# Kernel tuning notes

Hardware: AMD Instinct MI355X
Metric: run time of the kernel (lower is better)

## Reference

```python
import jax, jax.numpy as jnp
import numpy as np

NUM_USERS = 100000
NUM_ITEMS = 50000
EMBED_DIM = 64
N_LAYERS = 3
NUM_EDGES = 3276800  # avg user degree 32
BATCH = 16384


def setup_inputs() -> dict:
    key = jax.random.key(0)
    k0, k1, k2, k3, k4, k5 = jax.random.split(key, 6)
    rows = jax.random.randint(k0, (NUM_EDGES,), 0, NUM_USERS, dtype=jnp.int32)
    cols = jax.random.randint(k1, (NUM_EDGES,), 0, NUM_ITEMS, dtype=jnp.int32)
    user_table = jax.random.normal(k2, (NUM_USERS, EMBED_DIM), dtype=jnp.float32) * 0.1
    item_table = jax.random.normal(k3, (NUM_ITEMS, EMBED_DIM), dtype=jnp.float32) * 0.1
    user_indices = jax.random.randint(k4, (BATCH,), 0, NUM_USERS, dtype=jnp.int32)
    item_indices = jax.random.randint(k5, (BATCH,), 0, NUM_ITEMS, dtype=jnp.int32)
    return {
        "user_table": user_table,
        "item_table": item_table,
        "rows": rows,
        "cols": cols,
        "user_indices": user_indices,
        "item_indices": item_indices,
    }


def reference(user_table, item_table, rows, cols, user_indices, item_indices):
    # D^-1 A row-normalization of the binary bipartite adjacency:
    # normalized edge value for edge (u, i) is 1 / deg(u) (0 if isolated).
    ones = jnp.ones(rows.shape, dtype=user_table.dtype)
    deg = jax.ops.segment_sum(ones, rows, num_segments=NUM_USERS)
    inv_deg = jnp.where(deg > 0, 1.0 / deg, 0.0)
    vals = inv_deg[rows]  # [E]

    u = user_table  # [U, D] (unused by propagation in the original too)
    it = item_table  # [I, D]
    for _ in range(N_LAYERS):
        # u = A @ it  (SpMM via gather + segment-sum over destination users)
        u = jax.ops.segment_sum(vals[:, None] * it[cols], rows, num_segments=NUM_USERS)
        # it = A^T @ u
        it = jax.ops.segment_sum(vals[:, None] * u[rows], cols, num_segments=NUM_ITEMS)

    scores = jnp.sum(u[user_indices] * it[item_indices], axis=-1)  # [B]
    return jax.nn.sigmoid(scores)
```

## Files before the change

kernel.cpp:

```cpp
#include <hip/hip_runtime.h>
#include <math.h>

#define NUM_USERS 100000
#define NUM_ITEMS 50000
#define EMBED     64
#define NUM_EDGES 3276800
#define BATCH     16384
#define CAP       10752
#define NBUCK     391
#define NBUCK_I   391
#define P1_EDGES  16384
#define P1_THREADS 512
#define CVT_BLOCKS 1563

typedef _Float16 half8 __attribute__((ext_vector_type(8)));

__global__ void prep_kernel(const float* __restrict__ itab, _Float16* __restrict__ it16,
                            int* __restrict__ curzero,
                            _Float16* __restrict__ w16) {
    int b = blockIdx.x;
    if (b < CVT_BLOCKS) {
        int i = b * 256 + threadIdx.x;
        if (i < NUM_ITEMS * EMBED / 8) {
            const float4* p = (const float4*)itab + 2 * i;
            float4 a = p[0], c = p[1];
            half8 o;
            o[0] = (_Float16)a.x; o[1] = (_Float16)a.y; o[2] = (_Float16)a.z; o[3] = (_Float16)a.w;
            o[4] = (_Float16)c.x; o[5] = (_Float16)c.y; o[6] = (_Float16)c.z; o[7] = (_Float16)c.w;
            ((half8*)it16)[i] = o;
        }
    } else if (b == CVT_BLOCKS) {
        for (int k = threadIdx.x; k < 800; k += 256) curzero[k] = 0;
    } else {
        int i = threadIdx.x;
        if (i < 64) w16[(long long)NUM_USERS * EMBED + i] = (_Float16)0.f;
        else if (i < 128) it16[(long long)NUM_ITEMS * EMBED + (i - 64)] = (_Float16)0.f;
    }
}

__global__ void __launch_bounds__(P1_THREADS)
pass1_kernel(const int* __restrict__ rows, const int* __restrict__ cols,
             int* __restrict__ ucur, int* __restrict__ icur,
             int* __restrict__ rec_u, int* __restrict__ rec_i) {
    __shared__ int hu[400], hi[400], gu[400], gi[400];
    __shared__ int lbase[400], lcur[400];
    __shared__ int sc[512];
    __shared__ int recbuf[P1_EDGES];
    int t = threadIdx.x;
    long long e0 = (long long)blockIdx.x * P1_EDGES;

    int er[32], ec[32];
    #pragma unroll
    for (int q = 0; q < 32; ++q) {
        er[q] = rows[e0 + t + q * P1_THREADS];
        ec[q] = cols[e0 + t + q * P1_THREADS];
    }

    for (int i = t; i < 400; i += P1_THREADS) { hu[i] = 0; hi[i] = 0; }
    __syncthreads();
    #pragma unroll
    for (int q = 0; q < 32; ++q) {
        atomicAdd(&hu[er[q] >> 8], 1);
        atomicAdd(&hi[ec[q] >> 7], 1);
    }
    __syncthreads();
    for (int i = t; i < 400; i += P1_THREADS) {
        int vr = (hu[i] + 15) & ~15;
        gu[i] = vr ? atomicAdd(&ucur[i], vr) : 0;
        vr = (hi[i] + 15) & ~15;
        gi[i] = vr ? atomicAdd(&icur[i], vr) : 0;
    }

    __syncthreads();
    sc[t] = (t < 400) ? hu[t] : 0;
    __syncthreads();
    for (int o = 1; o < 512; o <<= 1) {
        int x = (t >= o) ? sc[t - o] : 0; __syncthreads();
        sc[t] += x; __syncthreads();
    }
    if (t < 400) { lbase[t] = sc[t] - hu[t]; lcur[t] = 0; }
    __syncthreads();
    #pragma unroll
    for (int q = 0; q < 32; ++q) {
        int b = er[q] >> 8;
        int p = lbase[b] + atomicAdd(&lcur[b], 1);
        recbuf[p] = (ec[q] << 8) | (er[q] & 255);
    }
    __syncthreads();
    sc[t] = (t < 400) ? ((hu[t] + 15) & ~15) : 0;
    __syncthreads();
    for (int o = 1; o < 512; o <<= 1) {
        int x = (t >= o) ? sc[t - o] : 0; __syncthreads();
        sc[t] += x; __syncthreads();
    }
    int total = sc[511];
    for (int o4 = t * 4; o4 < total; o4 += P1_THREADS * 4) {
        int lo = 0, hi_ = 399;
        while (lo < hi_) { int mid = (lo + hi_) >> 1; if (sc[mid] > o4) hi_ = mid; else lo = mid + 1; }
        int b = lo;
        int v = hu[b];
        int vr = (v + 15) & ~15;
        int j = o4 - (sc[b] - vr);
        int gpos = gu[b] + j;
        if (gpos + 3 < CAP) {
            int4 val;
            val.x = (j + 0 < v) ? recbuf[lbase[b] + j + 0] : -1;
            val.y = (j + 1 < v) ? recbuf[lbase[b] + j + 1] : -1;
            val.z = (j + 2 < v) ? recbuf[lbase[b] + j + 2] : -1;
            val.w = (j + 3 < v) ? recbuf[lbase[b] + j + 3] : -1;
            *(int4*)(rec_u + (long long)b * CAP + gpos) = val;
        } else {
            for (int k = 0; k < 4; ++k)
                if (gpos + k < CAP)
                    rec_u[(long long)b * CAP + gpos + k] = (j + k < v) ? recbuf[lbase[b] + j + k] : -1;
        }
    }

    __syncthreads();
    sc[t] = (t < 400) ? hi[t] : 0;
    __syncthreads();
    for (int o = 1; o < 512; o <<= 1) {
        int x = (t >= o) ? sc[t - o] : 0; __syncthreads();
        sc[t] += x; __syncthreads();
    }
    if (t < 400) { lbase[t] = sc[t] - hi[t]; lcur[t] = 0; }
    __syncthreads();
    #pragma unroll
    for (int q = 0; q < 32; ++q) {
        int b = ec[q] >> 7;
        int p = lbase[b] + atomicAdd(&lcur[b], 1);
        recbuf[p] = (er[q] << 7) | (ec[q] & 127);
    }
    __syncthreads();
    sc[t] = (t < 400) ? ((hi[t] + 15) & ~15) : 0;
    __syncthreads();
    for (int o = 1; o < 512; o <<= 1) {
        int x = (t >= o) ? sc[t - o] : 0; __syncthreads();
        sc[t] += x; __syncthreads();
    }
    total = sc[511];
    for (int o4 = t * 4; o4 < total; o4 += P1_THREADS * 4) {
        int lo = 0, hi_ = 399;
        while (lo < hi_) { int mid = (lo + hi_) >> 1; if (sc[mid] > o4) hi_ = mid; else lo = mid + 1; }
        int b = lo;
        int v = hi[b];
        int vr = (v + 15) & ~15;
        int j = o4 - (sc[b] - vr);
        int gpos = gi[b] + j;
        if (gpos + 3 < CAP) {
            int4 val;
            val.x = (j + 0 < v) ? recbuf[lbase[b] + j + 0] : -1;
            val.y = (j + 1 < v) ? recbuf[lbase[b] + j + 1] : -1;
            val.z = (j + 2 < v) ? recbuf[lbase[b] + j + 2] : -1;
            val.w = (j + 3 < v) ? recbuf[lbase[b] + j + 3] : -1;
            *(int4*)(rec_i + (long long)b * CAP + gpos) = val;
        } else {
            for (int k = 0; k < 4; ++k)
                if (gpos + k < CAP)
                    rec_i[(long long)b * CAP + gpos + k] = (j + k < v) ? recbuf[lbase[b] + j + k] : -1;
        }
    }
}

template <int VBITS>
__device__ __forceinline__ void pass2_body(int* __restrict__ rec, const int* __restrict__ cur,
                                           int* __restrict__ deg, int* __restrict__ off,
                                           float* __restrict__ inv32, int ncap, int b,
                                           int* buf, int* h, int* ex, int* cnt, int* sc) {
    const int V = 1 << VBITS, M = V - 1;
    int t = threadIdx.x;
    long long s = (long long)b * CAP;
    int n = cur[b]; if (n > CAP) n = CAP;
    for (int i = t; i < n; i += 256) buf[i] = rec[s + i];
    if (t < V) { h[t] = 0; cnt[t] = 0; }
    __syncthreads();
    for (int i = t; i < n; i += 256) {
        int r = buf[i];
        if (r != -1) atomicAdd(&h[r & M], 1);
    }
    __syncthreads();
    if (t < V) sc[t] = h[t];
    __syncthreads();
    for (int o = 1; o < V; o <<= 1) {
        int x = (t >= o && t < V) ? sc[t - o] : 0;
        __syncthreads();
        if (t < V) sc[t] += x;
        __syncthreads();
    }
    if (t < V) {
        ex[t] = sc[t] - h[t];
        int id = b * V + t;
        if (id < ncap) {
            int v = h[t];
            deg[id] = v;
            off[id] = (int)(s + ex[t]);
            if (inv32) inv32[id] = v ? 1.0f / (float)v : 0.0f;
        }
    }
    __syncthreads();
    for (int i = t; i < n; i += 256) {
        int r = buf[i];
        if (r == -1) continue;
        int k = r & M;
        int rnk = atomicAdd(&cnt[k], 1);
        rec[s + ex[k] + rnk] = (int)(((unsigned)r) >> VBITS);
    }
}

__global__ void __launch_bounds__(256)
pass2_kernel(int* __restrict__ rec_u, const int* __restrict__ ucur,
             int* __restrict__ udeg, int* __restrict__ uoff, float* __restrict__ inv32,
             int* __restrict__ rec_i, const int* __restrict__ icur,
             int* __restrict__ ideg, int* __restrict__ ioff) {
    __shared__ int buf[CAP];
    __shared__ int h[256], ex[256], cnt[256], sc[256];
    if (blockIdx.x < NBUCK)
        pass2_body<8>(rec_u, ucur, udeg, uoff, inv32, NUM_USERS, blockIdx.x,
                      buf, h, ex, cnt, sc);
    else
        pass2_body<7>(rec_i, icur, ideg, ioff, (float*)nullptr, NUM_ITEMS,
                      blockIdx.x - NBUCK, buf, h, ex, cnt, sc);
}

__global__ void gather_u(const int* __restrict__ uoff, const int* __restrict__ udeg,
                         const int* __restrict__ csr_col, const float* __restrict__ inv32,
                         const _Float16* __restrict__ it, _Float16* __restrict__ w) {
    int row = blockIdx.x * 4 + (threadIdx.x >> 6);
    if (row >= NUM_USERS) return;
    int lane = threadIdx.x & 63;
    int slot = lane >> 3;
    int h    = lane & 7;
    int start = uoff[row];
    int end = start + udeg[row];
    half8 acc = {0, 0, 0, 0, 0, 0, 0, 0};
    for (int k = start; k < end; k += 32) {
        int e1 = end - 1;
        int i0 = k + slot, i1 = i0 + 8, i2 = i0 + 16, i3 = i0 + 24;
        int c0 = csr_col[i0 < e1 ? i0 : e1];
        int c1 = csr_col[i1 < e1 ? i1 : e1];
        int c2 = csr_col[i2 < e1 ? i2 : e1];
        int c3 = csr_col[i3 < e1 ? i3 : e1];
        c0 = i0 < end ? c0 : NUM_ITEMS;
        c1 = i1 < end ? c1 : NUM_ITEMS;
        c2 = i2 < end ? c2 : NUM_ITEMS;
        c3 = i3 < end ? c3 : NUM_ITEMS;
        half8 x0 = *(const half8*)(it + (long long)c0 * EMBED + (h << 3));
        half8 x1 = *(const half8*)(it + (long long)c1 * EMBED + (h << 3));
        half8 x2 = *(const half8*)(it + (long long)c2 * EMBED + (h << 3));
        half8 x3 = *(const half8*)(it + (long long)c3 * EMBED + (h << 3));
        acc += x0; acc += x1; acc += x2; acc += x3;
    }
    float f[8];
    #pragma unroll
    for (int j = 0; j < 8; ++j) {
        f[j] = (float)acc[j];
        f[j] += __shfl_xor(f[j], 8, 64);
        f[j] += __shfl_xor(f[j], 16, 64);
        f[j] += __shfl_xor(f[j], 32, 64);
    }
    if (lane < 8) {
        float v = inv32[row];
        float v2 = v * v;
        half8 ow;
        #pragma unroll
        for (int j = 0; j < 8; ++j) ow[j] = (_Float16)(f[j] * v2);
        *(half8*)(w + (long long)row * EMBED + (lane << 3)) = ow;
    }
}

__device__ __forceinline__ void gather_it_body(int col, int lane,
                                               const int* __restrict__ ioff,
                                               const int* __restrict__ ideg,
                                               const int* __restrict__ csc_row,
                                               const _Float16* __restrict__ w,
                                               _Float16* __restrict__ it) {
    int slot = lane >> 3;
    int h    = lane & 7;
    int start = ioff[col];
    int end = start + ideg[col];
    half8 acc = {0, 0, 0, 0, 0, 0, 0, 0};
    for (int k = start; k < end; k += 64) {
        int e1 = end - 1;
        int idx[8], r[8];
        #pragma unroll
        for (int q = 0; q < 8; ++q) {
            idx[q] = k + slot + q * 8;
            int safe = idx[q] < e1 ? idx[q] : e1;
            r[q] = csc_row[safe];
            r[q] = idx[q] < end ? r[q] : NUM_USERS;
        }
        half8 x[8];
        #pragma unroll
        for (int q = 0; q < 8; ++q)
            x[q] = *(const half8*)(w + (long long)r[q] * EMBED + (h << 3));
        #pragma unroll
        for (int q = 0; q < 8; ++q) acc += x[q];
    }
    float f[8];
    #pragma unroll
    for (int j = 0; j < 8; ++j) {
        f[j] = (float)acc[j];
        f[j] += __shfl_xor(f[j], 8, 64);
        f[j] += __shfl_xor(f[j], 16, 64);
        f[j] += __shfl_xor(f[j], 32, 64);
    }
    if (lane < 8) {
        half8 o;
        #pragma unroll
        for (int j = 0; j < 8; ++j) o[j] = (_Float16)f[j];
        *(half8*)(it + (long long)col * EMBED + (lane << 3)) = o;
    }
}

__global__ void gather_it(const int* __restrict__ ioff, const int* __restrict__ ideg,
                          const int* __restrict__ csc_row,
                          const _Float16* __restrict__ w, _Float16* __restrict__ it) {
    int col = blockIdx.x * 4 + (threadIdx.x >> 6);
    if (col >= NUM_ITEMS) return;
    gather_it_body(col, threadIdx.x & 63, ioff, ideg, csc_row, w, it);
}

__global__ void gather_it_batch(const int* __restrict__ ioff, const int* __restrict__ ideg,
                                const int* __restrict__ csc_row,
                                const _Float16* __restrict__ w, _Float16* __restrict__ it,
                                const int* __restrict__ iidx) {
    int b = blockIdx.x * 4 + (threadIdx.x >> 6);
    if (b >= BATCH) return;
    gather_it_body(iidx[b], threadIdx.x & 63, ioff, ideg, csc_row, w, it);
}

__global__ void score_kernel(const _Float16* __restrict__ w, const _Float16* __restrict__ it,
                             const int* __restrict__ udeg,
                             const int* __restrict__ uidx, const int* __restrict__ iidx,
                             float* __restrict__ out) {
    int wave_in_block = threadIdx.x >> 6;
    int lane = threadIdx.x & 63;
    int b = blockIdx.x * 4 + wave_in_block;
    if (b >= BATCH) return;
    int ui = uidx[b];
    int ii = iidx[b];
    float s = (float)w[(long long)ui * EMBED + lane] * (float)it[(long long)ii * EMBED + lane];
    #pragma unroll
    for (int off = 32; off > 0; off >>= 1)
        s += __shfl_down(s, off, 64);
    if (lane == 0) {
        s *= (float)udeg[ui];
        out[b] = 1.0f / (1.0f + expf(-s));
    }
}

extern "C" void kernel_launch(void* const* d_in, const int* in_sizes, int n_in,
                              void* d_out, int out_size, void* d_ws, size_t ws_size,
                              hipStream_t stream) {
    const float* item_table = (const float*)d_in[1];
    const int*   rows       = (const int*)d_in[2];
    const int*   cols       = (const int*)d_in[3];
    const int*   uidx       = (const int*)d_in[4];
    const int*   iidx       = (const int*)d_in[5];
    float* out = (float*)d_out;

    char* base = (char*)d_ws;
    int*   udeg  = (int*)(base + 0);
    int*   ideg  = (int*)(base +   400000);
    int*   uoff  = (int*)(base +   600000);
    int*   ioff  = (int*)(base +  1000000);
    float* inv32 = (float*)(base + 1200000);
    int*   ucur  = (int*)(base +  1600000);
    int*   icur  = (int*)(base +  1601600);
    int*   rec_u = (int*)(base +  1720320);
    int*   rec_i = (int*)(base + 18923520);
    _Float16* w16  = (_Float16*)(base + 36126720);
    _Float16* it16 = (_Float16*)(base + 48926848);

    prep_kernel<<<CVT_BLOCKS + 2, 256, 0, stream>>>(item_table, it16, ucur, w16);

    pass1_kernel<<<NUM_EDGES / P1_EDGES, P1_THREADS, 0, stream>>>(
        rows, cols, ucur, icur, rec_u, rec_i);
    pass2_kernel<<<NBUCK + NBUCK_I, 256, 0, stream>>>(rec_u, ucur, udeg, uoff, inv32,
                                                      rec_i, icur, ideg, ioff);

    const int ublocks = (NUM_USERS + 3) / 4;
    const int iblocks = (NUM_ITEMS + 3) / 4;
    for (int l = 0; l < 3; ++l) {
        gather_u<<<ublocks, 256, 0, stream>>>(uoff, udeg, rec_u, inv32, it16, w16);
        if (l < 2)
            gather_it<<<iblocks, 256, 0, stream>>>(ioff, ideg, rec_i, w16, it16);
        else
            gather_it_batch<<<BATCH / 4, 256, 0, stream>>>(ioff, ideg, rec_i, w16, it16, iidx);
    }

    score_kernel<<<BATCH / 4, 256, 0, stream>>>(w16, it16, udeg, uidx, iidx, out);
}
```

Baseline: 431.8 us.

## Split item embeddings into column halves and fuse final item gather with scoring

Stores the fp16 item table as two 32-wide halves, and runs the user gather twice, once per half. Each pass gathers a 3.2 MB working set that is more likely to stay in cache. The last-layer item gather is merged with the score computation, so the item rows for the batch are no longer written and re-read. The cost is twice as many user-gather launches and a second read of the CSR indices.

```diff
diff --git a/kernel.cpp b/kernel.cpp
--- a/kernel.cpp
+++ b/kernel.cpp
@@ -8,33 +8,37 @@
 #define BATCH     16384
 #define CAP       10752
 #define NBUCK     391
-#define NBUCK_I   391
 #define P1_EDGES  16384
 #define P1_THREADS 512
-#define CVT_BLOCKS 1563
+#define CVT_GROUPS (NUM_ITEMS * 8)
+#define CVT_BLOCKS ((CVT_GROUPS + 255) / 256)
 
 typedef _Float16 half8 __attribute__((ext_vector_type(8)));
 
-__global__ void prep_kernel(const float* __restrict__ itab, _Float16* __restrict__ it16,
-                            int* __restrict__ curzero,
-                            _Float16* __restrict__ w16) {
+__global__ void prep_kernel(const float* __restrict__ itab,
+                            _Float16* __restrict__ it_lo, _Float16* __restrict__ it_hi,
+                            int* __restrict__ curzero, _Float16* __restrict__ w16) {
     int b = blockIdx.x;
     if (b < CVT_BLOCKS) {
         int i = b * 256 + threadIdx.x;
-        if (i < NUM_ITEMS * EMBED / 8) {
+        if (i < CVT_GROUPS) {
+            int row = i >> 3, g = i & 7;
             const float4* p = (const float4*)itab + 2 * i;
             float4 a = p[0], c = p[1];
             half8 o;
             o[0] = (_Float16)a.x; o[1] = (_Float16)a.y; o[2] = (_Float16)a.z; o[3] = (_Float16)a.w;
             o[4] = (_Float16)c.x; o[5] = (_Float16)c.y; o[6] = (_Float16)c.z; o[7] = (_Float16)c.w;
-            ((half8*)it16)[i] = o;
+            _Float16* dst = (g < 4) ? (it_lo + (long long)row * 32 + g * 8)
+                                    : (it_hi + (long long)row * 32 + (g - 4) * 8);
+            *(half8*)dst = o;
         }
     } else if (b == CVT_BLOCKS) {
         for (int k = threadIdx.x; k < 800; k += 256) curzero[k] = 0;
     } else {
         int i = threadIdx.x;
-        if (i < 64) w16[(long long)NUM_USERS * EMBED + i] = (_Float16)0.f;
-        else if (i < 128) it16[(long long)NUM_ITEMS * EMBED + (i - 64)] = (_Float16)0.f;
+        if (i < 32) it_lo[(long long)NUM_ITEMS * 32 + i] = (_Float16)0.f;
+        else if (i < 64) it_hi[(long long)NUM_ITEMS * 32 + (i - 32)] = (_Float16)0.f;
+        else if (i < 128) w16[(long long)NUM_USERS * EMBED + (i - 64)] = (_Float16)0.f;
     }
 }
 
@@ -222,20 +226,21 @@
                       blockIdx.x - NBUCK, buf, h, ex, cnt, sc);
 }
 
-__global__ void gather_u(const int* __restrict__ uoff, const int* __restrict__ udeg,
-                         const int* __restrict__ csr_col, const float* __restrict__ inv32,
-                         const _Float16* __restrict__ it, _Float16* __restrict__ w) {
+__global__ void gather_u_half(const int* __restrict__ uoff, const int* __restrict__ udeg,
+                              const int* __restrict__ csr_col, const float* __restrict__ inv32,
+                              const _Float16* __restrict__ itH,
+                              _Float16* __restrict__ w, int halfofs) {
     int row = blockIdx.x * 4 + (threadIdx.x >> 6);
     if (row >= NUM_USERS) return;
     int lane = threadIdx.x & 63;
-    int slot = lane >> 3;
-    int h    = lane & 7;
+    int slot = lane >> 2;
+    int d    = lane & 3;
     int start = uoff[row];
     int end = start + udeg[row];
     half8 acc = {0, 0, 0, 0, 0, 0, 0, 0};
-    for (int k = start; k < end; k += 32) {
+    for (int k = start; k < end; k += 64) {
         int e1 = end - 1;
-        int i0 = k + slot, i1 = i0 + 8, i2 = i0 + 16, i3 = i0 + 24;
+        int i0 = k + slot, i1 = i0 + 16, i2 = i0 + 32, i3 = i0 + 48;
         int c0 = csr_col[i0 < e1 ? i0 : e1];
         int c1 = csr_col[i1 < e1 ? i1 : e1];
         int c2 = csr_col[i2 < e1 ? i2 : e1];
@@ -244,36 +249,37 @@
         c1 = i1 < end ? c1 : NUM_ITEMS;
         c2 = i2 < end ? c2 : NUM_ITEMS;
         c3 = i3 < end ? c3 : NUM_ITEMS;
-        half8 x0 = *(const half8*)(it + (long long)c0 * EMBED + (h << 3));
-        half8 x1 = *(const half8*)(it + (long long)c1 * EMBED + (h << 3));
-        half8 x2 = *(const half8*)(it + (long long)c2 * EMBED + (h << 3));
-        half8 x3 = *(const half8*)(it + (long long)c3 * EMBED + (h << 3));
+        half8 x0 = *(const half8*)(itH + (long long)c0 * 32 + (d << 3));
+        half8 x1 = *(const half8*)(itH + (long long)c1 * 32 + (d << 3));
+        half8 x2 = *(const half8*)(itH + (long long)c2 * 32 + (d << 3));
+        half8 x3 = *(const half8*)(itH + (long long)c3 * 32 + (d << 3));
         acc += x0; acc += x1; acc += x2; acc += x3;
     }
     float f[8];
     #pragma unroll
     for (int j = 0; j < 8; ++j) {
         f[j] = (float)acc[j];
+        f[j] += __shfl_xor(f[j], 4, 64);
         f[j] += __shfl_xor(f[j], 8, 64);
         f[j] += __shfl_xor(f[j], 16, 64);
         f[j] += __shfl_xor(f[j], 32, 64);
     }
-    if (lane < 8) {
+    if (lane < 4) {
         float v = inv32[row];
         float v2 = v * v;
         half8 ow;
         #pragma unroll
         for (int j = 0; j < 8; ++j) ow[j] = (_Float16)(f[j] * v2);
-        *(half8*)(w + (long long)row * EMBED + (lane << 3)) = ow;
-    }
-}
-
-__device__ __forceinline__ void gather_it_body(int col, int lane,
-                                               const int* __restrict__ ioff,
-                                               const int* __restrict__ ideg,
-                                               const int* __restrict__ csc_row,
-                                               const _Float16* __restrict__ w,
-                                               _Float16* __restrict__ it) {
+        *(half8*)(w + (long long)row * EMBED + halfofs + (lane << 3)) = ow;
+    }
+}
+
+__global__ void gather_it(const int* __restrict__ ioff, const int* __restrict__ ideg,
+                          const int* __restrict__ csc_row, const _Float16* __restrict__ w,
+                          _Float16* __restrict__ it_lo, _Float16* __restrict__ it_hi) {
+    int col = blockIdx.x * 4 + (threadIdx.x >> 6);
+    if (col >= NUM_ITEMS) return;
+    int lane = threadIdx.x & 63;
     int slot = lane >> 3;
     int h    = lane & 7;
     int start = ioff[col];
@@ -308,43 +314,62 @@
         half8 o;
         #pragma unroll
         for (int j = 0; j < 8; ++j) o[j] = (_Float16)f[j];
-        *(half8*)(it + (long long)col * EMBED + (lane << 3)) = o;
-    }
-}
-
-__global__ void gather_it(const int* __restrict__ ioff, const int* __restrict__ ideg,
-                          const int* __restrict__ csc_row,
-                          const _Float16* __restrict__ w, _Float16* __restrict__ it) {
-    int col = blockIdx.x * 4 + (threadIdx.x >> 6);
-    if (col >= NUM_ITEMS) return;
-    gather_it_body(col, threadIdx.x & 63, ioff, ideg, csc_row, w, it);
-}
-
-__global__ void gather_it_batch(const int* __restrict__ ioff, const int* __restrict__ ideg,
-                                const int* __restrict__ csc_row,
-                                const _Float16* __restrict__ w, _Float16* __restrict__ it,
-                                const int* __restrict__ iidx) {
+        if (lane < 4)
+            *(half8*)(it_lo + (long long)col * 32 + (lane << 3)) = o;
+        else
+            *(half8*)(it_hi + (long long)col * 32 + ((lane - 4) << 3)) = o;
+    }
+}
+
+__global__ void batch_score(const int* __restrict__ ioff, const int* __restrict__ ideg,
+                            const int* __restrict__ csc_row, const _Float16* __restrict__ w,
+                            const int* __restrict__ udeg,
+                            const int* __restrict__ uidx, const int* __restrict__ iidx,
+                            float* __restrict__ out) {
     int b = blockIdx.x * 4 + (threadIdx.x >> 6);
     if (b >= BATCH) return;
-    gather_it_body(iidx[b], threadIdx.x & 63, ioff, ideg, csc_row, w, it);
-}
-
-__global__ void score_kernel(const _Float16* __restrict__ w, const _Float16* __restrict__ it,
-                             const int* __restrict__ udeg,
-                             const int* __restrict__ uidx, const int* __restrict__ iidx,
-                             float* __restrict__ out) {
-    int wave_in_block = threadIdx.x >> 6;
     int lane = threadIdx.x & 63;
-    int b = blockIdx.x * 4 + wave_in_block;
-    if (b >= BATCH) return;
+    int col = iidx[b];
+    int slot = lane >> 3;
+    int h    = lane & 7;
+    int start = ioff[col];
+    int end = start + ideg[col];
+    half8 acc = {0, 0, 0, 0, 0, 0, 0, 0};
+    for (int k = start; k < end; k += 64) {
+        int e1 = end - 1;
+        int idx[8], r[8];
+        #pragma unroll
+        for (int q = 0; q < 8; ++q) {
+            idx[q] = k + slot + q * 8;
+            int safe = idx[q] < e1 ? idx[q] : e1;
+            r[q] = csc_row[safe];
+            r[q] = idx[q] < end ? r[q] : NUM_USERS;
+        }
+        half8 x[8];
+        #pragma unroll
+        for (int q = 0; q < 8; ++q)
+            x[q] = *(const half8*)(w + (long long)r[q] * EMBED + (h << 3));
+        #pragma unroll
+        for (int q = 0; q < 8; ++q) acc += x[q];
+    }
+    float f[8];
+    #pragma unroll
+    for (int j = 0; j < 8; ++j) {
+        f[j] = (float)acc[j];
+        f[j] += __shfl_xor(f[j], 8, 64);
+        f[j] += __shfl_xor(f[j], 16, 64);
+        f[j] += __shfl_xor(f[j], 32, 64);
+    }
     int ui = uidx[b];
-    int ii = iidx[b];
-    float s = (float)w[(long long)ui * EMBED + lane] * (float)it[(long long)ii * EMBED + lane];
-    #pragma unroll
-    for (int off = 32; off > 0; off >>= 1)
-        s += __shfl_down(s, off, 64);
+    half8 wv = *(const half8*)(w + (long long)ui * EMBED + (h << 3));
+    float p = 0.f;
+    #pragma unroll
+    for (int j = 0; j < 8; ++j) p += f[j] * (float)wv[j];
+    p += __shfl_xor(p, 1, 64);
+    p += __shfl_xor(p, 2, 64);
+    p += __shfl_xor(p, 4, 64);
     if (lane == 0) {
-        s *= (float)udeg[ui];
+        float s = p * (float)udeg[ui];
         out[b] = 1.0f / (1.0f + expf(-s));
     }
 }
@@ -369,25 +394,25 @@
     int*   icur  = (int*)(base +  1601600);
     int*   rec_u = (int*)(base +  1720320);
     int*   rec_i = (int*)(base + 18923520);
-    _Float16* w16  = (_Float16*)(base + 36126720);
-    _Float16* it16 = (_Float16*)(base + 48926848);
-
-    prep_kernel<<<CVT_BLOCKS + 2, 256, 0, stream>>>(item_table, it16, ucur, w16);
+    _Float16* w16   = (_Float16*)(base + 36126720);
+    _Float16* it_lo = (_Float16*)(base + 48926848);
+    _Float16* it_hi = (_Float16*)(base + 52126912);
+
+    prep_kernel<<<CVT_BLOCKS + 2, 256, 0, stream>>>(item_table, it_lo, it_hi, ucur, w16);
 
     pass1_kernel<<<NUM_EDGES / P1_EDGES, P1_THREADS, 0, stream>>>(
         rows, cols, ucur, icur, rec_u, rec_i);
-    pass2_kernel<<<NBUCK + NBUCK_I, 256, 0, stream>>>(rec_u, ucur, udeg, uoff, inv32,
-                                                      rec_i, icur, ideg, ioff);
+    pass2_kernel<<<NBUCK * 2, 256, 0, stream>>>(rec_u, ucur, udeg, uoff, inv32,
+                                                rec_i, icur, ideg, ioff);
 
     const int ublocks = (NUM_USERS + 3) / 4;
     const int iblocks = (NUM_ITEMS + 3) / 4;
     for (int l = 0; l < 3; ++l) {
-        gather_u<<<ublocks, 256, 0, stream>>>(uoff, udeg, rec_u, inv32, it16, w16);
+        gather_u_half<<<ublocks, 256, 0, stream>>>(uoff, udeg, rec_u, inv32, it_lo, w16, 0);
+        gather_u_half<<<ublocks, 256, 0, stream>>>(uoff, udeg, rec_u, inv32, it_hi, w16, 32);
         if (l < 2)
-            gather_it<<<iblocks, 256, 0, stream>>>(ioff, ideg, rec_i, w16, it16);
-        else
-            gather_it_batch<<<BATCH / 4, 256, 0, stream>>>(ioff, ideg, rec_i, w16, it16, iidx);
-    }
-
-    score_kernel<<<BATCH / 4, 256, 0, stream>>>(w16, it16, udeg, uidx, iidx, out);
-}
+            gather_it<<<iblocks, 256, 0, stream>>>(ioff, ideg, rec_i, w16, it_lo, it_hi);
+    }
+    batch_score<<<BATCH / 4, 256, 0, stream>>>(ioff, ideg, rec_i, w16, udeg,
+                                               uidx, iidx, out);
+}
```

Result: slower. 517.7 us (+19.9%).
